# Kernel optimization log

Hardware: AMD Instinct MI355X
Metric: run time of the kernel (lower is better)

The kernel has to match this reference:

```python
import jax, jax.numpy as jnp
import numpy as np

N, F_IN, F_OUT = 8192, 512, 256

def setup_inputs() -> dict:
    key = jax.random.key(0)
    kx, kW, ka = jax.random.split(key, 3)
    x = jax.random.normal(kx, (N, F_IN), dtype=jnp.float32)
    adj = jnp.ones((N, N), dtype=jnp.float32)  # accepted but unused by the original forward
    # nn.Linear(in, out, bias=False) stores weight as [out, in]
    W = jax.random.normal(kW, (F_OUT, F_IN), dtype=jnp.float32) * 0.02
    # nn.Linear(2*out, 1, bias=False) -> attention vector of length 2*F_OUT
    a = jax.random.normal(ka, (2 * F_OUT,), dtype=jnp.float32) * 0.02
    return {"x": x, "adj": adj, "W": W, "a": a}

def reference(x, adj, W, a):
    # h = W(x): [N, F_OUT]
    h = x @ W.T
    # Original concatenates [h_i, h_j] for all pairs (O(N^2 * 2F) memory) and
    # applies linear a. Since a is linear, e_ij = a1.h_i + a2.h_j -> broadcast add.
    a_src, a_dst = a[:F_OUT], a[F_OUT:]
    e = (h @ a_src)[:, None] + (h @ a_dst)[None, :]  # [N, N]
    attention = jax.nn.softmax(e, axis=1)             # row-wise over neighbors j
    h_prime = attention @ h                           # [N, F_OUT]
    return h_prime
```

## Files before the change

kernel.cpp:

```cpp
#include <hip/hip_runtime.h>
#include <math.h>

#define NN 8192
#define FIN 512
#define FOUT 256


__global__ __launch_bounds__(256) void compute_g(const float* __restrict__ W,
                                                 const float* __restrict__ a_dst,
                                                 float* __restrict__ g) {
    __shared__ float red[4][64];
    const int tid = threadIdx.x;
    const int kl = tid & 63;
    const int cp = tid >> 6;
    const int k = blockIdx.x * 64 + kl;
    float s = 0.f;
    #pragma unroll 8
    for (int c = cp * 64; c < cp * 64 + 64; ++c)
        s = fmaf(W[(size_t)c * FIN + k], a_dst[c], s);
    red[cp][kl] = s;
    __syncthreads();
    if (cp == 0) g[k] = red[0][kl] + red[1][kl] + red[2][kl] + red[3][kl];
}

__global__ __launch_bounds__(256) void rowdot_xg(const float* __restrict__ x,
                                                 const float* __restrict__ g,
                                                 float* __restrict__ d) {
    __shared__ float gs[FIN];
    const int tid = threadIdx.x;
    if (tid < 128) ((float4*)gs)[tid] = ((const float4*)g)[tid];
    __syncthreads();
    const int lane = tid & 63;
    const int wave = tid >> 6;
    const int row = blockIdx.x * 4 + wave;
    const float4* xr = (const float4*)(x + (size_t)row * FIN);
    float4 x0 = xr[lane * 2], x1 = xr[lane * 2 + 1];
    float4 g0 = ((const float4*)gs)[lane * 2], g1 = ((const float4*)gs)[lane * 2 + 1];
    float s = x0.x * g0.x + x0.y * g0.y + x0.z * g0.z + x0.w * g0.w
            + x1.x * g1.x + x1.y * g1.y + x1.z * g1.z + x1.w * g1.w;
    #pragma unroll
    for (int off = 32; off; off >>= 1) s += __shfl_down(s, off);
    if (lane == 0) d[row] = s;
}

__global__ __launch_bounds__(1024) void softmax_stats(const float* __restrict__ d,
                                                      float* __restrict__ stats,
                                                      float* __restrict__ u) {
    __shared__ float red[16];
    const int tid = threadIdx.x;
    const int lane = tid & 63;
    const int wid = tid >> 6;

    if (tid < FIN) u[tid] = 0.f;

    const float4* dp = (const float4*)d + (size_t)tid * 2;
    float4 v0 = dp[0], v1 = dp[1];

    float m = fmaxf(fmaxf(fmaxf(v0.x, v0.y), fmaxf(v0.z, v0.w)),
                    fmaxf(fmaxf(v1.x, v1.y), fmaxf(v1.z, v1.w)));
    #pragma unroll
    for (int off = 32; off; off >>= 1) m = fmaxf(m, __shfl_xor(m, off));
    if (lane == 0) red[wid] = m;
    __syncthreads();
    if (tid == 0) {
        float mm = red[0];
        #pragma unroll
        for (int i = 1; i < 16; ++i) mm = fmaxf(mm, red[i]);
        red[0] = mm;
    }
    __syncthreads();
    const float M = red[0];
    __syncthreads();

    float s = expf(v0.x - M) + expf(v0.y - M) + expf(v0.z - M) + expf(v0.w - M)
            + expf(v1.x - M) + expf(v1.y - M) + expf(v1.z - M) + expf(v1.w - M);
    #pragma unroll
    for (int off = 32; off; off >>= 1) s += __shfl_xor(s, off);
    if (lane == 0) red[wid] = s;
    __syncthreads();
    if (tid == 0) {
        float ss = 0.f;
        #pragma unroll
        for (int i = 0; i < 16; ++i) ss += red[i];
        stats[0] = M;
        stats[1] = ss;
    }
}

__global__ __launch_bounds__(512) void weighted_colsum(const float* __restrict__ x,
                                                       const float* __restrict__ d,
                                                       const float* __restrict__ stats,
                                                       float* __restrict__ u) {
    __shared__ float w[128];
    const int tid = threadIdx.x;
    const int r0 = blockIdx.x * 128;
    const float M = stats[0];
    if (tid < 128) w[tid] = expf(d[r0 + tid] - M);
    __syncthreads();
    float acc = 0.f;
    #pragma unroll 8
    for (int j = 0; j < 128; ++j)
        acc = fmaf(w[j], x[(size_t)(r0 + j) * FIN + tid], acc);
    atomicAdd(&u[tid], acc);
}

__global__ __launch_bounds__(256) void compute_v(const float* __restrict__ W,
                                                 const float* __restrict__ u,
                                                 const float* __restrict__ stats,
                                                 float* __restrict__ vs) {
    __shared__ float us[FIN];
    const int tid = threadIdx.x;
    if (tid < 128) ((float4*)us)[tid] = ((const float4*)u)[tid];
    __syncthreads();
    const int lane = tid & 63;
    const int wave = tid >> 6;
    const int c = blockIdx.x * 4 + wave;
    const float4* wr = (const float4*)(W + (size_t)c * FIN);
    float4 w0 = wr[lane * 2], w1 = wr[lane * 2 + 1];
    float4 u0 = ((const float4*)us)[lane * 2], u1 = ((const float4*)us)[lane * 2 + 1];
    float s = w0.x * u0.x + w0.y * u0.y + w0.z * u0.z + w0.w * u0.w
            + w1.x * u1.x + w1.y * u1.y + w1.z * u1.z + w1.w * u1.w;
    #pragma unroll
    for (int off = 32; off; off >>= 1) s += __shfl_down(s, off);
    if (lane == 0) vs[c] = s / stats[1];
}

__global__ __launch_bounds__(256) void broadcast_out(const float* __restrict__ vs,
                                                     float* __restrict__ out) {
    const int idx = blockIdx.x * 256 + threadIdx.x;
    float4 vv = ((const float4*)vs)[idx & 63];
    ((float4*)out)[idx] = vv;
}

extern "C" void kernel_launch(void* const* d_in, const int* in_sizes, int n_in,
                              void* d_out, int out_size, void* d_ws, size_t ws_size,
                              hipStream_t stream) {
    const float* x = (const float*)d_in[0];
    const float* W = (const float*)d_in[2];
    const float* a = (const float*)d_in[3];
    float* out = (float*)d_out;

    float* ws    = (float*)d_ws;
    float* dvec  = ws;
    float* stats = ws + NN;
    float* g     = ws + NN + 16;
    float* u     = ws + NN + 16 + 512;
    float* vs    = ws + NN + 16 + 1024;

    compute_g<<<8, 256, 0, stream>>>(W, a + FOUT, g);
    rowdot_xg<<<NN / 4, 256, 0, stream>>>(x, g, dvec);
    softmax_stats<<<1, 1024, 0, stream>>>(dvec, stats, u);
    weighted_colsum<<<NN / 128, 512, 0, stream>>>(x, dvec, stats, u);
    compute_v<<<FOUT / 4, 256, 0, stream>>>(W, u, stats, vs);
    broadcast_out<<<(NN * FOUT / 4) / 256, 256, 0, stream>>>(vs, out);
}
```

Baseline: 330.2 us.

## Fuse row-dot, softmax stats and weighted column sum into one online-softmax pass

Merges the x·g row dot product, the global softmax statistics and the exp-weighted column sum of x into a single kernel. Each of 64 blocks computes a local max, sum and partial column sum, and a new combine kernel rescales and merges them, online-softmax style. This drops two launches, the second read of x and the single-block stats kernel, and replaces the atomics with per-block partials. In exchange only 64 blocks cover 8192 rows, which may underuse the GPU's compute units, and the x rows are re-read from cache inside the block.

```diff
diff --git a/kernel.cpp b/kernel.cpp
--- a/kernel.cpp
+++ b/kernel.cpp
@@ -4,6 +4,7 @@
 #define NN 8192
 #define FIN 512
 #define FOUT 256
+#define NBLK 64
 
 
 __global__ __launch_bounds__(256) void compute_g(const float* __restrict__ W,
@@ -23,106 +24,117 @@
     if (cp == 0) g[k] = red[0][kl] + red[1][kl] + red[2][kl] + red[3][kl];
 }
 
-__global__ __launch_bounds__(256) void rowdot_xg(const float* __restrict__ x,
-                                                 const float* __restrict__ g,
-                                                 float* __restrict__ d) {
+__global__ __launch_bounds__(512) void fused_pass(const float* __restrict__ x,
+                                                  const float* __restrict__ g,
+                                                  float* __restrict__ pm,
+                                                  float* __restrict__ ps,
+                                                  float* __restrict__ pu) {
     __shared__ float gs[FIN];
+    __shared__ float ds[128];
+    __shared__ float wred[8];
     const int tid = threadIdx.x;
+    const int lane = tid & 63;
+    const int wave = tid >> 6;
+    const int r0 = blockIdx.x * 128;
+
     if (tid < 128) ((float4*)gs)[tid] = ((const float4*)g)[tid];
     __syncthreads();
-    const int lane = tid & 63;
-    const int wave = tid >> 6;
-    const int row = blockIdx.x * 4 + wave;
-    const float4* xr = (const float4*)(x + (size_t)row * FIN);
-    float4 x0 = xr[lane * 2], x1 = xr[lane * 2 + 1];
-    float4 g0 = ((const float4*)gs)[lane * 2], g1 = ((const float4*)gs)[lane * 2 + 1];
-    float s = x0.x * g0.x + x0.y * g0.y + x0.z * g0.z + x0.w * g0.w
-            + x1.x * g1.x + x1.y * g1.y + x1.z * g1.z + x1.w * g1.w;
-    #pragma unroll
-    for (int off = 32; off; off >>= 1) s += __shfl_down(s, off);
-    if (lane == 0) d[row] = s;
-}
 
-__global__ __launch_bounds__(1024) void softmax_stats(const float* __restrict__ d,
-                                                      float* __restrict__ stats,
-                                                      float* __restrict__ u) {
-    __shared__ float red[16];
-    const int tid = threadIdx.x;
-    const int lane = tid & 63;
-    const int wid = tid >> 6;
+    const float4* gv = (const float4*)gs;
+    float4 g0 = gv[lane], g1 = gv[lane + 64];
 
-    if (tid < FIN) u[tid] = 0.f;
-
-    const float4* dp = (const float4*)d + (size_t)tid * 2;
-    float4 v0 = dp[0], v1 = dp[1];
-
-    float m = fmaxf(fmaxf(fmaxf(v0.x, v0.y), fmaxf(v0.z, v0.w)),
-                    fmaxf(fmaxf(v1.x, v1.y), fmaxf(v1.z, v1.w)));
-    #pragma unroll
-    for (int off = 32; off; off >>= 1) m = fmaxf(m, __shfl_xor(m, off));
-    if (lane == 0) red[wid] = m;
-    __syncthreads();
-    if (tid == 0) {
-        float mm = red[0];
+    float lmax = -1e30f;
+    #pragma unroll 4
+    for (int rr = 0; rr < 16; ++rr) {
+        const int j = wave * 16 + rr;
+        const float4* xr = (const float4*)(x + (size_t)(r0 + j) * FIN);
+        float4 x0 = xr[lane], x1 = xr[lane + 64];
+        float s = x0.x * g0.x + x0.y * g0.y + x0.z * g0.z + x0.w * g0.w
+                + x1.x * g1.x + x1.y * g1.y + x1.z * g1.z + x1.w * g1.w;
         #pragma unroll
-        for (int i = 1; i < 16; ++i) mm = fmaxf(mm, red[i]);
-        red[0] = mm;
+        for (int off = 32; off; off >>= 1) s += __shfl_xor(s, off);
+        if (lane == 0) ds[j] = s;
+        lmax = fmaxf(lmax, s);
     }
-    __syncthreads();
-    const float M = red[0];
+    if (lane == 0) wred[wave] = lmax;
     __syncthreads();
 
-    float s = expf(v0.x - M) + expf(v0.y - M) + expf(v0.z - M) + expf(v0.w - M)
-            + expf(v1.x - M) + expf(v1.y - M) + expf(v1.z - M) + expf(v1.w - M);
+    float m_b = wred[0];
     #pragma unroll
-    for (int off = 32; off; off >>= 1) s += __shfl_xor(s, off);
-    if (lane == 0) red[wid] = s;
+    for (int i = 1; i < 8; ++i) m_b = fmaxf(m_b, wred[i]);
+
+    if (tid < 128) ds[tid] = expf(ds[tid] - m_b);
     __syncthreads();
-    if (tid == 0) {
-        float ss = 0.f;
+
+    if (wave == 0) {
+        float s = ds[lane] + ds[lane + 64];
         #pragma unroll
-        for (int i = 0; i < 16; ++i) ss += red[i];
-        stats[0] = M;
-        stats[1] = ss;
+        for (int off = 32; off; off >>= 1) s += __shfl_xor(s, off);
+        if (lane == 0) {
+            ps[blockIdx.x] = s;
+            pm[blockIdx.x] = m_b;
+        }
     }
-}
 
-__global__ __launch_bounds__(512) void weighted_colsum(const float* __restrict__ x,
-                                                       const float* __restrict__ d,
-                                                       const float* __restrict__ stats,
-                                                       float* __restrict__ u) {
-    __shared__ float w[128];
-    const int tid = threadIdx.x;
-    const int r0 = blockIdx.x * 128;
-    const float M = stats[0];
-    if (tid < 128) w[tid] = expf(d[r0 + tid] - M);
-    __syncthreads();
     float acc = 0.f;
     #pragma unroll 8
     for (int j = 0; j < 128; ++j)
-        acc = fmaf(w[j], x[(size_t)(r0 + j) * FIN + tid], acc);
-    atomicAdd(&u[tid], acc);
+        acc = fmaf(ds[j], x[(size_t)(r0 + j) * FIN + tid], acc);
+    pu[(size_t)blockIdx.x * FIN + tid] = acc;
+}
+
+__global__ __launch_bounds__(512) void combine(const float* __restrict__ pm,
+                                               const float* __restrict__ ps,
+                                               const float* __restrict__ pu,
+                                               float* __restrict__ u_scaled) {
+    __shared__ float m_s[NBLK];
+    __shared__ float sc[NBLK];
+    __shared__ float Ss;
+    const int tid = threadIdx.x;
+    if (tid < NBLK) m_s[tid] = pm[tid];
+    __syncthreads();
+
+    float M = m_s[0];
+    #pragma unroll 8
+    for (int i = 1; i < NBLK; ++i) M = fmaxf(M, m_s[i]);
+
+    if (tid < NBLK) sc[tid] = expf(m_s[tid] - M);
+    __syncthreads();
+
+    if (tid < 64) {
+        float s = ps[tid] * sc[tid];
+        #pragma unroll
+        for (int off = 32; off; off >>= 1) s += __shfl_xor(s, off);
+        if (tid == 0) Ss = s;
+    }
+    __syncthreads();
+
+    float acc = 0.f;
+    #pragma unroll 8
+    for (int b = 0; b < NBLK; ++b)
+        acc = fmaf(sc[b], pu[(size_t)b * FIN + tid], acc);
+    u_scaled[tid] = acc / Ss;
 }
 
 __global__ __launch_bounds__(256) void compute_v(const float* __restrict__ W,
-                                                 const float* __restrict__ u,
-                                                 const float* __restrict__ stats,
+                                                 const float* __restrict__ u_scaled,
                                                  float* __restrict__ vs) {
     __shared__ float us[FIN];
     const int tid = threadIdx.x;
-    if (tid < 128) ((float4*)us)[tid] = ((const float4*)u)[tid];
+    if (tid < 128) ((float4*)us)[tid] = ((const float4*)u_scaled)[tid];
     __syncthreads();
     const int lane = tid & 63;
     const int wave = tid >> 6;
     const int c = blockIdx.x * 4 + wave;
     const float4* wr = (const float4*)(W + (size_t)c * FIN);
-    float4 w0 = wr[lane * 2], w1 = wr[lane * 2 + 1];
-    float4 u0 = ((const float4*)us)[lane * 2], u1 = ((const float4*)us)[lane * 2 + 1];
+    const float4* uv = (const float4*)us;
+    float4 w0 = wr[lane], w1 = wr[lane + 64];
+    float4 u0 = uv[lane], u1 = uv[lane + 64];
     float s = w0.x * u0.x + w0.y * u0.y + w0.z * u0.z + w0.w * u0.w
             + w1.x * u1.x + w1.y * u1.y + w1.z * u1.z + w1.w * u1.w;
     #pragma unroll
-    for (int off = 32; off; off >>= 1) s += __shfl_down(s, off);
-    if (lane == 0) vs[c] = s / stats[1];
+    for (int off = 32; off; off >>= 1) s += __shfl_xor(s, off);
+    if (lane == 0) vs[c] = s;
 }
 
 __global__ __launch_bounds__(256) void broadcast_out(const float* __restrict__ vs,
@@ -140,17 +152,17 @@
     const float* a = (const float*)d_in[3];
     float* out = (float*)d_out;
 
-    float* ws    = (float*)d_ws;
-    float* dvec  = ws;
-    float* stats = ws + NN;
-    float* g     = ws + NN + 16;
-    float* u     = ws + NN + 16 + 512;
-    float* vs    = ws + NN + 16 + 1024;
+    float* ws   = (float*)d_ws;
+    float* g    = ws;
+    float* pm   = ws + 512;
+    float* ps   = ws + 512 + 64;
+    float* pu   = ws + 1024;
+    float* u    = ws + 1024 + NBLK * FIN;
+    float* vs   = u + FIN;
 
     compute_g<<<8, 256, 0, stream>>>(W, a + FOUT, g);
-    rowdot_xg<<<NN / 4, 256, 0, stream>>>(x, g, dvec);
-    softmax_stats<<<1, 1024, 0, stream>>>(dvec, stats, u);
-    weighted_colsum<<<NN / 128, 512, 0, stream>>>(x, dvec, stats, u);
-    compute_v<<<FOUT / 4, 256, 0, stream>>>(W, u, stats, vs);
+    fused_pass<<<NBLK, 512, 0, stream>>>(x, g, pm, ps, pu);
+    combine<<<1, 512, 0, stream>>>(pm, ps, pu, u);
+    compute_v<<<FOUT / 4, 256, 0, stream>>>(W, u, vs);
     broadcast_out<<<(NN * FOUT / 4) / 256, 256, 0, stream>>>(vs, out);
 }
```

After: 336.1 us. No clear change (+1.8%).
